# Kernel optimization log

Measured on AMD Instinct MI355X. Metric: run time of the kernel, lower is better.

## Reference

```python
import jax, jax.numpy as jnp
import numpy as np

THRESH = 0.5
LENS = 0.5
DECAY = 0.5
CFG_FC = [256, 256, 256]
IN_SIZE = 1
OUT_SIZE = 10
T = 784 // IN_SIZE  # stride == input_size


def make_mask(dim, c_min, c_max, min_dc, max_dc, phase_shift_max, T=784):
    mask = []
    dc_steps = np.linspace(min_dc, max_dc, dim)
    cycles = np.linspace(c_min, c_max, dim)
    phase_shifts = np.linspace(0, int(phase_shift_max * c_max), dim)
    for cycle, dc, ps in zip(cycles, dc_steps, phase_shifts):
        cycle = int(np.ceil(cycle))
        on_length = int(np.ceil(dc * cycle))
        off_length = cycle - on_length
        pattern = [1] * on_length + [0] * off_length
        ps = int(np.round(ps))
        pattern = pattern[-ps:] + pattern[:-ps] if ps > 0 else pattern
        full_pattern = pattern * (T // cycle) + pattern[: T % cycle]
        mask.append(full_pattern)
    return jnp.asarray(np.array(mask, dtype=np.float32))  # [dim, T]


MASK1 = make_mask(CFG_FC[0], 4, 8, 0.1, 0.9, 0.5, T)
MASK2 = make_mask(CFG_FC[1], 4, 8, 0.1, 0.9, 0.5, T)
MASK3 = make_mask(CFG_FC[2], 4, 8, 0.1, 0.9, 0.5, T)


def act_fun(x):
    return (x > THRESH).astype(x.dtype)


def mem_update(x, mem, spike, mask):
    # mask: [H] broadcast over batch
    pre_mem = mem
    new_mem = mem * DECAY * (1.0 - spike) + x
    mem = jnp.where(mask == 0, pre_mem, new_mem)
    spike = act_fun(mem) * mask
    return mem, spike


def setup_inputs() -> dict:
    key = jax.random.key(0)
    ks = jax.random.split(key, 14)
    def lin(k, out_d, in_d):
        s = 1.0 / np.sqrt(in_d)
        return jax.random.uniform(k, (out_d, in_d), jnp.float32, -s, s)
    def bia(k, out_d, in_d):
        s = 1.0 / np.sqrt(in_d)
        return jax.random.uniform(k, (out_d,), jnp.float32, -s, s)
    H1, H2, H3 = CFG_FC
    return {
        "x": jax.random.uniform(ks[0], (512, 784), jnp.float32),
        "w_i2h1": lin(ks[1], H1, IN_SIZE), "b_i2h1": bia(ks[2], H1, IN_SIZE),
        "w_h2h1": lin(ks[3], H1, H1), "b_h2h1": bia(ks[4], H1, H1),
        "w_i2h2": lin(ks[5], H2, H1), "b_i2h2": bia(ks[6], H2, H1),
        "w_h2h2": lin(ks[7], H2, H2), "b_h2h2": bia(ks[8], H2, H2),
        "w_i2h3": lin(ks[9], H3, H2), "b_i2h3": bia(ks[10], H3, H2),
        "w_h2o3": lin(ks[11], OUT_SIZE, H3), "b_h2o3": bia(ks[12], OUT_SIZE, H3),
    }


def _build_x_seq(x):
    # replicate the torch slicing: start = step*stride, clamp to last window
    D = x.shape[1]
    starts = np.arange(T) * IN_SIZE
    starts = np.where(starts < T - IN_SIZE, starts, D - IN_SIZE)
    idx = starts[:, None] + np.arange(IN_SIZE)  # [T, in]
    x_seq = x[:, idx]                            # [N, T, in]
    return jnp.transpose(x_seq, (1, 0, 2))       # [T, N, in]


def reference(x, w_i2h1, b_i2h1, w_h2h1, b_h2h1, w_i2h2, b_i2h2,
              w_h2h2, b_h2h2, w_i2h3, b_i2h3, w_h2o3, b_h2o3):
    N = x.shape[0]
    H1, H2, H3 = CFG_FC
    x_seq = _build_x_seq(x)                       # [T, N, in]
    m1 = MASK1.T                                  # [T, H1]
    m2 = MASK2.T
    m3 = MASK3.T

    init = (jnp.zeros((N, H1)), jnp.zeros((N, H1)),
            jnp.zeros((N, H2)), jnp.zeros((N, H2)),
            jnp.zeros((N, H3)), jnp.zeros((N, H3)),
            jnp.zeros((N, OUT_SIZE)))

    def step(carry, inp):
        mem1, spk1, mem2, spk2, mem3, spk3, out_sum = carry
        xt, mk1, mk2, mk3 = inp
        h1 = xt @ w_i2h1.T + b_i2h1 + spk1 @ w_h2h1.T + b_h2h1
        mem1, spk1 = mem_update(h1, mem1, spk1, mk1)
        h2 = spk1 @ w_i2h2.T + b_i2h2 + spk2 @ w_h2h2.T + b_h2h2
        mem2, spk2 = mem_update(h2, mem2, spk2, mk2)
        h3 = spk2 @ w_i2h3.T + b_i2h3
        mem3, spk3 = mem_update(h3, mem3, spk3, mk3)
        out = spk3 @ w_h2o3.T + b_h2o3
        return (mem1, spk1, mem2, spk2, mem3, spk3, out_sum + out), None

    (final, _) = jax.lax.scan(step, init, (x_seq, m1, m2, m3))
    out_sum = final[-1]
    return out_sum / T
```

## Files before the change

### kernel.cpp

```cpp
#include <hip/hip_runtime.h>
#include <stdint.h>

#define T_STEPS 784
#define H 256
#define NBLK 512
#define NTHR 256

typedef unsigned long long u64;

__device__ __forceinline__ void mask_params(int j, int& c, int& on, int& ps) {
    const double stepc = (8.0 - 4.0) / 255.0;
    const double stepd = (0.9 - 0.1) / 255.0;
    const double stepp = 4.0 / 255.0;
    double cyc = (j == 255) ? 8.0 : __dadd_rn(__dmul_rn((double)j, stepc), 4.0);
    c = (int)ceil(cyc);
    double dc  = (j == 255) ? 0.9 : __dadd_rn(__dmul_rn((double)j, stepd), 0.1);
    on = (int)ceil(__dmul_rn(dc, (double)c));
    double psd = (j == 255) ? 4.0 : __dmul_rn((double)j, stepp);
    ps = (int)rint(psd);
}

__device__ __forceinline__ void acc_add(const float4& w, float4& a) {
    a.x += w.x; a.y += w.y; a.z += w.z; a.w += w.w;
}

__device__ __forceinline__ void consume_pair(const char* __restrict__ bX,
                                             const char* __restrict__ bY,
                                             u64 m, int l16,
                                             float4& aX, float4& aY) {
    int n = __popcll(m);
    while (n >= 8) {
        int k0=__builtin_ctzll(m); m&=m-1; int k1=__builtin_ctzll(m); m&=m-1;
        int k2=__builtin_ctzll(m); m&=m-1; int k3=__builtin_ctzll(m); m&=m-1;
        int k4=__builtin_ctzll(m); m&=m-1; int k5=__builtin_ctzll(m); m&=m-1;
        int k6=__builtin_ctzll(m); m&=m-1; int k7=__builtin_ctzll(m); m&=m-1;
        float4 x0 = *(const float4*)(bX + (k0<<10) + l16);
        float4 x1 = *(const float4*)(bX + (k1<<10) + l16);
        float4 x2 = *(const float4*)(bX + (k2<<10) + l16);
        float4 x3 = *(const float4*)(bX + (k3<<10) + l16);
        float4 x4 = *(const float4*)(bX + (k4<<10) + l16);
        float4 x5 = *(const float4*)(bX + (k5<<10) + l16);
        float4 x6 = *(const float4*)(bX + (k6<<10) + l16);
        float4 x7 = *(const float4*)(bX + (k7<<10) + l16);
        float4 y0 = *(const float4*)(bY + (k0<<10) + l16);
        float4 y1 = *(const float4*)(bY + (k1<<10) + l16);
        float4 y2 = *(const float4*)(bY + (k2<<10) + l16);
        float4 y3 = *(const float4*)(bY + (k3<<10) + l16);
        float4 y4 = *(const float4*)(bY + (k4<<10) + l16);
        float4 y5 = *(const float4*)(bY + (k5<<10) + l16);
        float4 y6 = *(const float4*)(bY + (k6<<10) + l16);
        float4 y7 = *(const float4*)(bY + (k7<<10) + l16);
        acc_add(x0, aX); acc_add(x1, aX); acc_add(x2, aX); acc_add(x3, aX);
        acc_add(x4, aX); acc_add(x5, aX); acc_add(x6, aX); acc_add(x7, aX);
        acc_add(y0, aY); acc_add(y1, aY); acc_add(y2, aY); acc_add(y3, aY);
        acc_add(y4, aY); acc_add(y5, aY); acc_add(y6, aY); acc_add(y7, aY);
        n -= 8;
    }
    if (n & 4) {
        int k0=__builtin_ctzll(m); m&=m-1; int k1=__builtin_ctzll(m); m&=m-1;
        int k2=__builtin_ctzll(m); m&=m-1; int k3=__builtin_ctzll(m); m&=m-1;
        float4 x0 = *(const float4*)(bX + (k0<<10) + l16);
        float4 x1 = *(const float4*)(bX + (k1<<10) + l16);
        float4 x2 = *(const float4*)(bX + (k2<<10) + l16);
        float4 x3 = *(const float4*)(bX + (k3<<10) + l16);
        float4 y0 = *(const float4*)(bY + (k0<<10) + l16);
        float4 y1 = *(const float4*)(bY + (k1<<10) + l16);
        float4 y2 = *(const float4*)(bY + (k2<<10) + l16);
        float4 y3 = *(const float4*)(bY + (k3<<10) + l16);
        acc_add(x0, aX); acc_add(x1, aX); acc_add(x2, aX); acc_add(x3, aX);
        acc_add(y0, aY); acc_add(y1, aY); acc_add(y2, aY); acc_add(y3, aY);
    }
    if (n & 2) {
        int k0=__builtin_ctzll(m); m&=m-1; int k1=__builtin_ctzll(m); m&=m-1;
        float4 x0 = *(const float4*)(bX + (k0<<10) + l16);
        float4 x1 = *(const float4*)(bX + (k1<<10) + l16);
        float4 y0 = *(const float4*)(bY + (k0<<10) + l16);
        float4 y1 = *(const float4*)(bY + (k1<<10) + l16);
        acc_add(x0, aX); acc_add(x1, aX);
        acc_add(y0, aY); acc_add(y1, aY);
    }
    if (n & 1) {
        int k0 = __builtin_ctzll(m);
        float4 x0 = *(const float4*)(bX + (k0<<10) + l16);
        float4 y0 = *(const float4*)(bY + (k0<<10) + l16);
        acc_add(x0, aX); acc_add(y0, aY);
    }
}

__device__ __forceinline__ void upd(float& mem, float& sp, float h, int mbit) {
    float nm = fmaf(mem * 0.5f, (1.0f - sp), h);
    mem = mbit ? nm : mem;
    sp  = (mbit && (mem > 0.5f)) ? 1.0f : 0.0f;
}

__global__ __launch_bounds__(256)
void prep_transpose(const float* __restrict__ w1, const float* __restrict__ w2a,
                    const float* __restrict__ w2b, const float* __restrict__ w3,
                    float* __restrict__ ws)
{
    __shared__ float tile[64][65];
    const int bid = blockIdx.x;
    const int m  = bid >> 4;
    const int kt = (bid >> 2) & 3;
    const int jt = bid & 3;
    const float* src = (m == 0) ? w1 : (m == 1) ? w2a : (m == 2) ? w2b : w3;
    float* dst = ws + (size_t)m * H * H;
    const int tid = threadIdx.x;
    const int c = tid & 63, r4 = tid >> 6;
    #pragma unroll
    for (int rr = 0; rr < 16; rr++) {
        int r = r4 * 16 + rr;
        tile[r][c] = src[(size_t)(jt * 64 + r) * H + kt * 64 + c];
    }
    __syncthreads();
    #pragma unroll
    for (int rr = 0; rr < 16; rr++) {
        int r = r4 * 16 + rr;
        dst[(size_t)(kt * 64 + r) * H + jt * 64 + c] = tile[c][r];
    }
}

__global__ __launch_bounds__(NTHR, 2)
void srnn_kernel(const float* __restrict__ x,
                 const float* __restrict__ w_i2h1, const float* __restrict__ b_i2h1,
                 const float* __restrict__ b_h2h1,
                 const float* __restrict__ b_i2h2, const float* __restrict__ b_h2h2,
                 const float* __restrict__ b_i2h3,
                 const float* __restrict__ w_h2o3, const float* __restrict__ b_h2o3,
                 const float* __restrict__ ws,
                 float* __restrict__ out)
{
    const int tid  = threadIdx.x;
    const int lane = tid & 63;
    const int w    = tid >> 6;
    const int j    = tid;
    const int l16  = lane * 16;
    const int s    = blockIdx.x;

    const char* wt1  = (const char*)ws + (0 << 18) + (w << 16);
    const char* wt2a = (const char*)ws + (1 << 18) + (w << 16);
    const char* wt2b = (const char*)ws + (2 << 18) + (w << 16);
    const char* wt3  = (const char*)ws + (3 << 18) + (w << 16);

    __shared__ float xls[T_STEPS];
    __shared__ float pexA[2][4][H];
    __shared__ float pexB[2][4][H];
    __shared__ float pexC[2][4][H];
    __shared__ float wred[4][10];

    for (int i = tid; i < T_STEPS; i += NTHR)
        xls[i] = x[(size_t)s * T_STEPS + i];

    int mc, mon, mps;
    mask_params(j, mc, mon, mps);
    int ph = (mc - (mps % mc)) % mc;

    const float bs1 = b_i2h1[j] + b_h2h1[j];
    const float bs2 = b_i2h2[j] + b_h2h2[j];
    const float bs3 = b_i2h3[j];
    const float wi1 = w_i2h1[j];

    float mem1 = 0.f, mem2 = 0.f, mem3 = 0.f;
    float sp1 = 0.f, sp2 = 0.f, sp3 = 0.f;
    u64 bal1 = 0ull, bal2 = 0ull;
    int mb_d1 = 0, mb_d2 = 0;
    float cnt = 0.f;

    __syncthreads();

    for (int sl = 0; sl < T_STEPS + 2; sl++) {
        const int par  = sl & 1;
        const int mbit = (ph < mon) ? 1 : 0;
        const bool runL1 = (sl < T_STEPS);
        const bool runL2 = (sl >= 1) && (sl <= T_STEPS);
        const bool runL3 = (sl >= 2);

        float4 accA = {0.f,0.f,0.f,0.f}, accB = {0.f,0.f,0.f,0.f}, accC = {0.f,0.f,0.f,0.f};
        consume_pair(wt1,  wt2a, bal1, l16, accA, accB);
        consume_pair(wt2b, wt3,  bal2, l16, accB, accC);
        if (runL1) ((float4*)pexA[par][w])[lane] = accA;
        if (runL2) ((float4*)pexB[par][w])[lane] = accB;
        if (runL3) ((float4*)pexC[par][w])[lane] = accC;
        __syncthreads();

        if (runL1) {
            float hs = (pexA[par][0][j] + pexA[par][1][j])
                     + (pexA[par][2][j] + pexA[par][3][j]);
            float h1 = hs + fmaf(xls[sl], wi1, bs1);
            upd(mem1, sp1, h1, mbit);
            bal1 = __ballot(sp1 != 0.0f);
        }
        if (runL2) {
            float hs = (pexB[par][0][j] + pexB[par][1][j])
                     + (pexB[par][2][j] + pexB[par][3][j]);
            upd(mem2, sp2, hs + bs2, mb_d1);
            bal2 = __ballot(sp2 != 0.0f);
        }
        if (runL3) {
            float hs = (pexC[par][0][j] + pexC[par][1][j])
                     + (pexC[par][2][j] + pexC[par][3][j]);
            upd(mem3, sp3, hs + bs3, mb_d2);
            cnt += sp3;
        }
        mb_d2 = mb_d1; mb_d1 = mbit;
        ph++; if (ph == mc) ph = 0;
    }

    #pragma unroll
    for (int i = 0; i < 10; i++) {
        float v = cnt * w_h2o3[i * H + j];
        for (int off = 32; off; off >>= 1) v += __shfl_down(v, off, 64);
        if (lane == 0) wred[w][i] = v;
    }
    __syncthreads();
    if (tid < 10) {
        float sum = wred[0][tid] + wred[1][tid] + wred[2][tid] + wred[3][tid];
        out[(size_t)s * 10 + tid] = sum / 784.0f + b_h2o3[tid];
    }
}

extern "C" void kernel_launch(void* const* d_in, const int* in_sizes, int n_in,
                              void* d_out, int out_size, void* d_ws, size_t ws_size,
                              hipStream_t stream) {
    (void)in_sizes; (void)n_in; (void)ws_size; (void)out_size;
    const float* x      = (const float*)d_in[0];
    const float* w_i2h1 = (const float*)d_in[1];
    const float* b_i2h1 = (const float*)d_in[2];
    const float* w_h2h1 = (const float*)d_in[3];
    const float* b_h2h1 = (const float*)d_in[4];
    const float* w_i2h2 = (const float*)d_in[5];
    const float* b_i2h2 = (const float*)d_in[6];
    const float* w_h2h2 = (const float*)d_in[7];
    const float* b_h2h2 = (const float*)d_in[8];
    const float* w_i2h3 = (const float*)d_in[9];
    const float* b_i2h3 = (const float*)d_in[10];
    const float* w_h2o3 = (const float*)d_in[11];
    const float* b_h2o3 = (const float*)d_in[12];
    float* ws = (float*)d_ws;

    prep_transpose<<<64, 256, 0, stream>>>(w_h2h1, w_i2h2, w_h2h2, w_i2h3, ws);
    srnn_kernel<<<NBLK, NTHR, 0, stream>>>(x,
        w_i2h1, b_i2h1, b_h2h1,
        b_i2h2, b_h2h2, b_i2h3,
        w_h2o3, b_h2o3, ws,
        (float*)d_out);
}
```

Measured before the change: 1.793 ms.

## Split recurrent matvec reduction across eight waves per block

Doubles the block to 512 threads, so each of 8 waves handles 32 input neurons (rows) instead of 64. Spike ballots are masked to the low 32 lanes, and the partial sums in shared memory are reduced over 8 slices. This is meant to shorten each timestep's serial sparse accumulation on the critical path. The cost is more shared-memory traffic, duplicated neuron state in the upper half-waves, and tighter register limits from launch_bounds(512,4), which risk spills.

```diff
diff --git a/kernel.cpp b/kernel.cpp
--- a/kernel.cpp
+++ b/kernel.cpp
@@ -4,9 +4,10 @@
 #define T_STEPS 784
 #define H 256
 #define NBLK 512
-#define NTHR 256
+#define NTHR 512
 
 typedef unsigned long long u64;
+typedef unsigned int u32;
 
 __device__ __forceinline__ void mask_params(int j, int& c, int& on, int& ps) {
     const double stepc = (8.0 - 4.0) / 255.0;
@@ -120,7 +121,7 @@
     }
 }
 
-__global__ __launch_bounds__(NTHR, 2)
+__global__ __launch_bounds__(NTHR, 4)
 void srnn_kernel(const float* __restrict__ x,
                  const float* __restrict__ w_i2h1, const float* __restrict__ b_i2h1,
                  const float* __restrict__ b_h2h1,
@@ -133,20 +134,20 @@
     const int tid  = threadIdx.x;
     const int lane = tid & 63;
     const int w    = tid >> 6;
-    const int j    = tid;
+    const int j    = w * 32 + (lane & 31);
     const int l16  = lane * 16;
     const int s    = blockIdx.x;
 
-    const char* wt1  = (const char*)ws + (0 << 18) + (w << 16);
-    const char* wt2a = (const char*)ws + (1 << 18) + (w << 16);
-    const char* wt2b = (const char*)ws + (2 << 18) + (w << 16);
-    const char* wt3  = (const char*)ws + (3 << 18) + (w << 16);
+    const char* wt1  = (const char*)ws + (0 << 18) + (w << 15);
+    const char* wt2a = (const char*)ws + (1 << 18) + (w << 15);
+    const char* wt2b = (const char*)ws + (2 << 18) + (w << 15);
+    const char* wt3  = (const char*)ws + (3 << 18) + (w << 15);
 
     __shared__ float xls[T_STEPS];
-    __shared__ float pexA[2][4][H];
-    __shared__ float pexB[2][4][H];
-    __shared__ float pexC[2][4][H];
-    __shared__ float wred[4][10];
+    __shared__ float pexA[2][8][H];
+    __shared__ float pexB[2][8][H];
+    __shared__ float pexC[2][8][H];
+    __shared__ float wred[8][10];
 
     for (int i = tid; i < T_STEPS; i += NTHR)
         xls[i] = x[(size_t)s * T_STEPS + i];
@@ -176,29 +177,35 @@
         const bool runL3 = (sl >= 2);
 
         float4 accA = {0.f,0.f,0.f,0.f}, accB = {0.f,0.f,0.f,0.f}, accC = {0.f,0.f,0.f,0.f};
-        consume_pair(wt1,  wt2a, bal1, l16, accA, accB);
-        consume_pair(wt2b, wt3,  bal2, l16, accB, accC);
+        consume_pair(wt1,  wt2a, bal1 & 0xFFFFFFFFull, l16, accA, accB);
+        consume_pair(wt2b, wt3,  bal2 & 0xFFFFFFFFull, l16, accB, accC);
         if (runL1) ((float4*)pexA[par][w])[lane] = accA;
         if (runL2) ((float4*)pexB[par][w])[lane] = accB;
         if (runL3) ((float4*)pexC[par][w])[lane] = accC;
         __syncthreads();
 
         if (runL1) {
-            float hs = (pexA[par][0][j] + pexA[par][1][j])
-                     + (pexA[par][2][j] + pexA[par][3][j]);
+            float hs = ((pexA[par][0][j] + pexA[par][1][j])
+                      + (pexA[par][2][j] + pexA[par][3][j]))
+                     + ((pexA[par][4][j] + pexA[par][5][j])
+                      + (pexA[par][6][j] + pexA[par][7][j]));
             float h1 = hs + fmaf(xls[sl], wi1, bs1);
             upd(mem1, sp1, h1, mbit);
             bal1 = __ballot(sp1 != 0.0f);
         }
         if (runL2) {
-            float hs = (pexB[par][0][j] + pexB[par][1][j])
-                     + (pexB[par][2][j] + pexB[par][3][j]);
+            float hs = ((pexB[par][0][j] + pexB[par][1][j])
+                      + (pexB[par][2][j] + pexB[par][3][j]))
+                     + ((pexB[par][4][j] + pexB[par][5][j])
+                      + (pexB[par][6][j] + pexB[par][7][j]));
             upd(mem2, sp2, hs + bs2, mb_d1);
             bal2 = __ballot(sp2 != 0.0f);
         }
         if (runL3) {
-            float hs = (pexC[par][0][j] + pexC[par][1][j])
-                     + (pexC[par][2][j] + pexC[par][3][j]);
+            float hs = ((pexC[par][0][j] + pexC[par][1][j])
+                      + (pexC[par][2][j] + pexC[par][3][j]))
+                     + ((pexC[par][4][j] + pexC[par][5][j])
+                      + (pexC[par][6][j] + pexC[par][7][j]));
             upd(mem3, sp3, hs + bs3, mb_d2);
             cnt += sp3;
         }
@@ -206,15 +213,18 @@
         ph++; if (ph == mc) ph = 0;
     }
 
+    float wo_i;
     #pragma unroll
     for (int i = 0; i < 10; i++) {
-        float v = cnt * w_h2o3[i * H + j];
-        for (int off = 32; off; off >>= 1) v += __shfl_down(v, off, 64);
+        wo_i = w_h2o3[i * H + j];
+        float v = cnt * wo_i;
+        for (int off = 16; off; off >>= 1) v += __shfl_down(v, off, 32);
         if (lane == 0) wred[w][i] = v;
     }
     __syncthreads();
     if (tid < 10) {
-        float sum = wred[0][tid] + wred[1][tid] + wred[2][tid] + wred[3][tid];
+        float sum = ((wred[0][tid] + wred[1][tid]) + (wred[2][tid] + wred[3][tid]))
+                  + ((wred[4][tid] + wred[5][tid]) + (wred[6][tid] + wred[7][tid]));
         out[(size_t)s * 10 + tid] = sum / 784.0f + b_h2o3[tid];
     }
 }
```

Result: faster. 1.731 ms (median of 2 runs) (-3.5%).

## Process two samples per block sharing weight-row loads via union spike masks

Applied to the files above, without the earlier changes.

Each block now handles two batch samples instead of one, halving the grid to 256 blocks. Weight rows are loaded once for the union of both samples' spike ballots and applied to each sample with per-sample 0/1 FMA factors. This amortizes weight loads and per-step barriers across two samples. In exchange it adds FMA work, more registers and shared memory, and fewer blocks, which may underfill the GPU's compute units and lengthen the serial step loop per block.

```diff
diff --git a/kernel.cpp b/kernel.cpp
--- a/kernel.cpp
+++ b/kernel.cpp
@@ -3,7 +3,7 @@
 
 #define T_STEPS 784
 #define H 256
-#define NBLK 512
+#define NBLK 256
 #define NTHR 256
 
 typedef unsigned long long u64;
@@ -20,20 +20,30 @@
     ps = (int)rint(psd);
 }
 
-__device__ __forceinline__ void acc_add(const float4& w, float4& a) {
-    a.x += w.x; a.y += w.y; a.z += w.z; a.w += w.w;
-}
-
-__device__ __forceinline__ void consume_pair(const char* __restrict__ bX,
-                                             const char* __restrict__ bY,
-                                             u64 m, int l16,
-                                             float4& aX, float4& aY) {
-    int n = __popcll(m);
+__device__ __forceinline__ void fmac4(float4& a, float f, const float4& w) {
+    a.x = fmaf(f, w.x, a.x); a.y = fmaf(f, w.y, a.y);
+    a.z = fmaf(f, w.z, a.z); a.w = fmaf(f, w.w, a.w);
+}
+
+#define SELF(m,k) ((((m) >> (k)) & 1ull) ? 1.0f : 0.0f)
+
+#define APPLY2(ki, xi, yi)                                         \
+    {   float f0 = SELF(m0, ki), f1 = SELF(m1, ki);                \
+        fmac4(aX0, f0, xi); fmac4(aX1, f1, xi);                    \
+        fmac4(aY0, f0, yi); fmac4(aY1, f1, yi); }
+
+__device__ __forceinline__ void consume_pair_2s(const char* __restrict__ bX,
+                                                const char* __restrict__ bY,
+                                                u64 m0, u64 m1, int l16,
+                                                float4& aX0, float4& aX1,
+                                                float4& aY0, float4& aY1) {
+    u64 u = m0 | m1;
+    int n = __popcll(u);
     while (n >= 8) {
-        int k0=__builtin_ctzll(m); m&=m-1; int k1=__builtin_ctzll(m); m&=m-1;
-        int k2=__builtin_ctzll(m); m&=m-1; int k3=__builtin_ctzll(m); m&=m-1;
-        int k4=__builtin_ctzll(m); m&=m-1; int k5=__builtin_ctzll(m); m&=m-1;
-        int k6=__builtin_ctzll(m); m&=m-1; int k7=__builtin_ctzll(m); m&=m-1;
+        int k0=__builtin_ctzll(u); u&=u-1; int k1=__builtin_ctzll(u); u&=u-1;
+        int k2=__builtin_ctzll(u); u&=u-1; int k3=__builtin_ctzll(u); u&=u-1;
+        int k4=__builtin_ctzll(u); u&=u-1; int k5=__builtin_ctzll(u); u&=u-1;
+        int k6=__builtin_ctzll(u); u&=u-1; int k7=__builtin_ctzll(u); u&=u-1;
         float4 x0 = *(const float4*)(bX + (k0<<10) + l16);
         float4 x1 = *(const float4*)(bX + (k1<<10) + l16);
         float4 x2 = *(const float4*)(bX + (k2<<10) + l16);
@@ -50,15 +60,15 @@
         float4 y5 = *(const float4*)(bY + (k5<<10) + l16);
         float4 y6 = *(const float4*)(bY + (k6<<10) + l16);
         float4 y7 = *(const float4*)(bY + (k7<<10) + l16);
-        acc_add(x0, aX); acc_add(x1, aX); acc_add(x2, aX); acc_add(x3, aX);
-        acc_add(x4, aX); acc_add(x5, aX); acc_add(x6, aX); acc_add(x7, aX);
-        acc_add(y0, aY); acc_add(y1, aY); acc_add(y2, aY); acc_add(y3, aY);
-        acc_add(y4, aY); acc_add(y5, aY); acc_add(y6, aY); acc_add(y7, aY);
+        APPLY2(k0, x0, y0); APPLY2(k1, x1, y1);
+        APPLY2(k2, x2, y2); APPLY2(k3, x3, y3);
+        APPLY2(k4, x4, y4); APPLY2(k5, x5, y5);
+        APPLY2(k6, x6, y6); APPLY2(k7, x7, y7);
         n -= 8;
     }
     if (n & 4) {
-        int k0=__builtin_ctzll(m); m&=m-1; int k1=__builtin_ctzll(m); m&=m-1;
-        int k2=__builtin_ctzll(m); m&=m-1; int k3=__builtin_ctzll(m); m&=m-1;
+        int k0=__builtin_ctzll(u); u&=u-1; int k1=__builtin_ctzll(u); u&=u-1;
+        int k2=__builtin_ctzll(u); u&=u-1; int k3=__builtin_ctzll(u); u&=u-1;
         float4 x0 = *(const float4*)(bX + (k0<<10) + l16);
         float4 x1 = *(const float4*)(bX + (k1<<10) + l16);
         float4 x2 = *(const float4*)(bX + (k2<<10) + l16);
@@ -67,23 +77,22 @@
         float4 y1 = *(const float4*)(bY + (k1<<10) + l16);
         float4 y2 = *(const float4*)(bY + (k2<<10) + l16);
         float4 y3 = *(const float4*)(bY + (k3<<10) + l16);
-        acc_add(x0, aX); acc_add(x1, aX); acc_add(x2, aX); acc_add(x3, aX);
-        acc_add(y0, aY); acc_add(y1, aY); acc_add(y2, aY); acc_add(y3, aY);
+        APPLY2(k0, x0, y0); APPLY2(k1, x1, y1);
+        APPLY2(k2, x2, y2); APPLY2(k3, x3, y3);
     }
     if (n & 2) {
-        int k0=__builtin_ctzll(m); m&=m-1; int k1=__builtin_ctzll(m); m&=m-1;
+        int k0=__builtin_ctzll(u); u&=u-1; int k1=__builtin_ctzll(u); u&=u-1;
         float4 x0 = *(const float4*)(bX + (k0<<10) + l16);
         float4 x1 = *(const float4*)(bX + (k1<<10) + l16);
         float4 y0 = *(const float4*)(bY + (k0<<10) + l16);
         float4 y1 = *(const float4*)(bY + (k1<<10) + l16);
-        acc_add(x0, aX); acc_add(x1, aX);
-        acc_add(y0, aY); acc_add(y1, aY);
+        APPLY2(k0, x0, y0); APPLY2(k1, x1, y1);
     }
     if (n & 1) {
-        int k0 = __builtin_ctzll(m);
-        float4 x0 = *(const float4*)(bX + (k0<<10) + l16);
-        float4 y0 = *(const float4*)(bY + (k0<<10) + l16);
-        acc_add(x0, aX); acc_add(y0, aY);
+        int k0 = __builtin_ctzll(u);
+        float4 x0 = *(const float4*)(bX + (k0<<10) + l16);
+        float4 y0 = *(const float4*)(bY + (k0<<10) + l16);
+        APPLY2(k0, x0, y0);
     }
 }
 
@@ -135,21 +144,23 @@
     const int w    = tid >> 6;
     const int j    = tid;
     const int l16  = lane * 16;
-    const int s    = blockIdx.x;
+    const int s0   = blockIdx.x * 2;
 
     const char* wt1  = (const char*)ws + (0 << 18) + (w << 16);
     const char* wt2a = (const char*)ws + (1 << 18) + (w << 16);
     const char* wt2b = (const char*)ws + (2 << 18) + (w << 16);
     const char* wt3  = (const char*)ws + (3 << 18) + (w << 16);
 
-    __shared__ float xls[T_STEPS];
-    __shared__ float pexA[2][4][H];
-    __shared__ float pexB[2][4][H];
-    __shared__ float pexC[2][4][H];
-    __shared__ float wred[4][10];
-
-    for (int i = tid; i < T_STEPS; i += NTHR)
-        xls[i] = x[(size_t)s * T_STEPS + i];
+    __shared__ float xls[2][T_STEPS];
+    __shared__ float pexA[2][2][4][H];
+    __shared__ float pexB[2][2][4][H];
+    __shared__ float pexC[2][2][4][H];
+    __shared__ float wred[4][2][10];
+
+    for (int i = tid; i < 2 * T_STEPS; i += NTHR) {
+        int sp = i / T_STEPS, t = i - sp * T_STEPS;
+        xls[sp][t] = x[(size_t)(s0 + sp) * T_STEPS + t];
+    }
 
     int mc, mon, mps;
     mask_params(j, mc, mon, mps);
@@ -160,11 +171,12 @@
     const float bs3 = b_i2h3[j];
     const float wi1 = w_i2h1[j];
 
-    float mem1 = 0.f, mem2 = 0.f, mem3 = 0.f;
-    float sp1 = 0.f, sp2 = 0.f, sp3 = 0.f;
-    u64 bal1 = 0ull, bal2 = 0ull;
+    float mem1[2] = {0.f,0.f}, mem2[2] = {0.f,0.f}, mem3[2] = {0.f,0.f};
+    float sp1 [2] = {0.f,0.f}, sp2 [2] = {0.f,0.f}, sp3 [2] = {0.f,0.f};
+    u64 b1s0 = 0ull, b1s1 = 0ull;
+    u64 b2s0 = 0ull, b2s1 = 0ull;
     int mb_d1 = 0, mb_d2 = 0;
-    float cnt = 0.f;
+    float cnt[2] = {0.f, 0.f};
 
     __syncthreads();
 
@@ -175,32 +187,58 @@
         const bool runL2 = (sl >= 1) && (sl <= T_STEPS);
         const bool runL3 = (sl >= 2);
 
-        float4 accA = {0.f,0.f,0.f,0.f}, accB = {0.f,0.f,0.f,0.f}, accC = {0.f,0.f,0.f,0.f};
-        consume_pair(wt1,  wt2a, bal1, l16, accA, accB);
-        consume_pair(wt2b, wt3,  bal2, l16, accB, accC);
-        if (runL1) ((float4*)pexA[par][w])[lane] = accA;
-        if (runL2) ((float4*)pexB[par][w])[lane] = accB;
-        if (runL3) ((float4*)pexC[par][w])[lane] = accC;
+        float4 aA0={0,0,0,0}, aA1={0,0,0,0}, aBa0={0,0,0,0}, aBa1={0,0,0,0};
+        float4 aBb0={0,0,0,0}, aBb1={0,0,0,0}, aC0={0,0,0,0}, aC1={0,0,0,0};
+        consume_pair_2s(wt1,  wt2a, b1s0, b1s1, l16, aA0, aA1, aBa0, aBa1);
+        consume_pair_2s(wt2b, wt3,  b2s0, b2s1, l16, aBb0, aBb1, aC0, aC1);
+        float4 aB0, aB1;
+        aB0.x = aBa0.x + aBb0.x; aB0.y = aBa0.y + aBb0.y;
+        aB0.z = aBa0.z + aBb0.z; aB0.w = aBa0.w + aBb0.w;
+        aB1.x = aBa1.x + aBb1.x; aB1.y = aBa1.y + aBb1.y;
+        aB1.z = aBa1.z + aBb1.z; aB1.w = aBa1.w + aBb1.w;
+        if (runL1) {
+            ((float4*)pexA[par][0][w])[lane] = aA0;
+            ((float4*)pexA[par][1][w])[lane] = aA1;
+        }
+        if (runL2) {
+            ((float4*)pexB[par][0][w])[lane] = aB0;
+            ((float4*)pexB[par][1][w])[lane] = aB1;
+        }
+        if (runL3) {
+            ((float4*)pexC[par][0][w])[lane] = aC0;
+            ((float4*)pexC[par][1][w])[lane] = aC1;
+        }
         __syncthreads();
 
         if (runL1) {
-            float hs = (pexA[par][0][j] + pexA[par][1][j])
-                     + (pexA[par][2][j] + pexA[par][3][j]);
-            float h1 = hs + fmaf(xls[sl], wi1, bs1);
-            upd(mem1, sp1, h1, mbit);
-            bal1 = __ballot(sp1 != 0.0f);
+            #pragma unroll
+            for (int sp = 0; sp < 2; sp++) {
+                float hs = (pexA[par][sp][0][j] + pexA[par][sp][1][j])
+                         + (pexA[par][sp][2][j] + pexA[par][sp][3][j]);
+                float h1 = hs + fmaf(xls[sp][sl], wi1, bs1);
+                upd(mem1[sp], sp1[sp], h1, mbit);
+            }
+            b1s0 = __ballot(sp1[0] != 0.0f);
+            b1s1 = __ballot(sp1[1] != 0.0f);
         }
         if (runL2) {
-            float hs = (pexB[par][0][j] + pexB[par][1][j])
-                     + (pexB[par][2][j] + pexB[par][3][j]);
-            upd(mem2, sp2, hs + bs2, mb_d1);
-            bal2 = __ballot(sp2 != 0.0f);
+            #pragma unroll
+            for (int sp = 0; sp < 2; sp++) {
+                float hs = (pexB[par][sp][0][j] + pexB[par][sp][1][j])
+                         + (pexB[par][sp][2][j] + pexB[par][sp][3][j]);
+                upd(mem2[sp], sp2[sp], hs + bs2, mb_d1);
+            }
+            b2s0 = __ballot(sp2[0] != 0.0f);
+            b2s1 = __ballot(sp2[1] != 0.0f);
         }
         if (runL3) {
-            float hs = (pexC[par][0][j] + pexC[par][1][j])
-                     + (pexC[par][2][j] + pexC[par][3][j]);
-            upd(mem3, sp3, hs + bs3, mb_d2);
-            cnt += sp3;
+            #pragma unroll
+            for (int sp = 0; sp < 2; sp++) {
+                float hs = (pexC[par][sp][0][j] + pexC[par][sp][1][j])
+                         + (pexC[par][sp][2][j] + pexC[par][sp][3][j]);
+                upd(mem3[sp], sp3[sp], hs + bs3, mb_d2);
+                cnt[sp] += sp3[sp];
+            }
         }
         mb_d2 = mb_d1; mb_d1 = mbit;
         ph++; if (ph == mc) ph = 0;
@@ -208,14 +246,20 @@
 
     #pragma unroll
     for (int i = 0; i < 10; i++) {
-        float v = cnt * w_h2o3[i * H + j];
-        for (int off = 32; off; off >>= 1) v += __shfl_down(v, off, 64);
-        if (lane == 0) wred[w][i] = v;
+        float wo_i = w_h2o3[i * H + j];
+        #pragma unroll
+        for (int sp = 0; sp < 2; sp++) {
+            float v = cnt[sp] * wo_i;
+            for (int off = 32; off; off >>= 1) v += __shfl_down(v, off, 64);
+            if (lane == 0) wred[w][sp][i] = v;
+        }
     }
     __syncthreads();
-    if (tid < 10) {
-        float sum = wred[0][tid] + wred[1][tid] + wred[2][tid] + wred[3][tid];
-        out[(size_t)s * 10 + tid] = sum / 784.0f + b_h2o3[tid];
+    if (tid < 20) {
+        int sp = tid / 10, i = tid % 10;
+        float sum = (wred[0][sp][i] + wred[1][sp][i])
+                  + (wred[2][sp][i] + wred[3][sp][i]);
+        out[(size_t)(s0 + sp) * 10 + i] = sum / 784.0f + b_h2o3[i];
     }
 }
 
```

Result: slower. 2.067 ms (+15.3%).
